# Kernel optimization log

Hardware: AMD Instinct MI355X
Metric: run time of the kernel (lower is better)

The kernel has to match this reference:

```python
import jax, jax.numpy as jnp
import numpy as np

B, S, D, H = 2, 2048, 1024, 16
HD = D // H
NEG = -10000.0


def setup_inputs() -> dict:
    key = jax.random.key(0)
    ks = jax.random.split(key, 9)
    # xavier-uniform-like scale for square d_model x d_model weights
    lim = float(np.sqrt(6.0 / (D + D)))
    mk_w = lambda k: jax.random.uniform(k, (D, D), jnp.float32, -lim, lim)
    return {
        "q": jax.random.normal(ks[0], (B, S, D), jnp.float32),
        "k": jax.random.normal(ks[1], (B, S, D), jnp.float32),
        "v": jax.random.normal(ks[2], (B, S, D), jnp.float32),
        "attn_mask": jax.random.randint(ks[3], (B, S), 0, 2, jnp.int32),
        "Wq": mk_w(ks[4]),
        "Wk": mk_w(ks[5]),
        "Wv": mk_w(ks[6]),
        "Wo": mk_w(ks[7]),
        "mask_future": 1,
    }


def reference(q, k, v, attn_mask, Wq, Wk, Wv, Wo, mask_future):
    # nn.Linear(bias=False): y = x @ W.T
    def split_heads(x, W):
        return (x @ W.T).reshape(B, S, H, HD).transpose(0, 2, 1, 3)  # [B,H,S,HD]

    qh = split_heads(q, Wq)
    kh = split_heads(k, Wk)
    vh = split_heads(v, Wv)

    scale = 1.0 / np.sqrt(HD)
    scores = jnp.einsum("bhld,bhsd->bhls", qh, kh) * scale  # [B,H,L,S]

    if mask_future:  # static python flag
        rows = jnp.arange(S)[:, None]
        cols = jnp.arange(S)[None, :]
        causal_bias = jnp.where(cols > rows, jnp.float32(NEG), jnp.float32(0.0))
        scores = scores + causal_bias

    # masked_fill(attn_mask == 0, -10000): sets score exactly to NEG (after bias add)
    pad = attn_mask[:, None, None, :]  # [B,1,1,S]
    scores = jnp.where(pad == 0, jnp.float32(NEG), scores)

    probs = jax.nn.softmax(scores, axis=-1)
    ctx = jnp.einsum("bhls,bhsd->bhld", probs, vh)  # [B,H,L,HD]
    ctx = ctx.transpose(0, 2, 1, 3).reshape(B, S, D)
    return ctx @ Wo.T
```

## Files before the change

kernel.cpp:

```cpp
#include <hip/hip_runtime.h>
#include <hip/hip_bf16.h>

typedef __attribute__((ext_vector_type(8))) short bf16x8;
typedef __attribute__((ext_vector_type(4))) short bf16x4;
typedef __attribute__((ext_vector_type(4))) float f32x4;

#define B_ 2
#define S_ 2048
#define D_ 1024
#define H_ 16
#define HD_ 64
#define M_ 4096
#define NEGV (-10000.0f)

#define NQ_ 4194304
#define NW_ 1048576

#if __has_builtin(__builtin_amdgcn_mfma_f32_16x16x16bf16_1k)
#define HAVE_MFMA16 1
#else
#define HAVE_MFMA16 0
#endif

static __device__ __forceinline__ unsigned short f2bf(float x) {
  __hip_bfloat16 h = __float2bfloat16(x);
  return *reinterpret_cast<unsigned short*>(&h);
}

static __device__ __forceinline__ bf16x8 cvt8(const float* p) {
  float4 a = *reinterpret_cast<const float4*>(p);
  float4 b = *reinterpret_cast<const float4*>(p + 4);
  bf16x8 r;
  r[0] = (short)f2bf(a.x); r[1] = (short)f2bf(a.y);
  r[2] = (short)f2bf(a.z); r[3] = (short)f2bf(a.w);
  r[4] = (short)f2bf(b.x); r[5] = (short)f2bf(b.y);
  r[6] = (short)f2bf(b.z); r[7] = (short)f2bf(b.w);
  return r;
}

static __device__ __forceinline__ void gl_lds16(const unsigned short* g, unsigned short* l) {
#if __has_builtin(__builtin_amdgcn_global_load_lds)
  __builtin_amdgcn_global_load_lds(
      (const __attribute__((address_space(1))) unsigned int*)g,
      (__attribute__((address_space(3))) unsigned int*)l, 16, 0, 0);
#else
  *reinterpret_cast<bf16x8*>(l) = *reinterpret_cast<const bf16x8*>(g);
#endif
}


__global__ __launch_bounds__(256) void cvt_all(const float* __restrict__ q,
                                               const float* __restrict__ k,
                                               const float* __restrict__ v,
                                               const float* __restrict__ wq,
                                               const float* __restrict__ wk,
                                               const float* __restrict__ wv,
                                               const float* __restrict__ wo,
                                               unsigned short* __restrict__ dst) {
  for (size_t c = (size_t)blockIdx.x * 256 + threadIdx.x; c < 2097152; c += (size_t)2048 * 256) {
    const size_t e = c * 8;
    const float* s;
    if (e < (size_t)NQ_)            s = q  + e;
    else if (e < (size_t)2 * NQ_)   s = k  + (e - (size_t)NQ_);
    else if (e < (size_t)3 * NQ_)   s = v  + (e - (size_t)2 * NQ_);
    else if (e < (size_t)3 * NQ_ + NW_)     s = wq + (e - (size_t)3 * NQ_);
    else if (e < (size_t)3 * NQ_ + 2 * NW_) s = wk + (e - (size_t)3 * NQ_ - NW_);
    else if (e < (size_t)3 * NQ_ + 3 * NW_) s = wv + (e - (size_t)3 * NQ_ - 2 * NW_);
    else                                    s = wo + (e - (size_t)3 * NQ_ - 3 * NW_);
    *reinterpret_cast<bf16x8*>(dst + e) = cvt8(s);
  }
}

template<bool HSPLIT>
static __device__ __forceinline__ void core_fast(const unsigned short* A,
                                                 const unsigned short* Bw,
                                                 unsigned short* Asm, unsigned short* Bsm,
                                                 int m0, int n0, f32x4 (*acc)[4]) {
  const int tid = threadIdx.x, lane = tid & 63, wid = tid >> 6;
  const int wm = wid >> 1, wn = wid & 1;
  const int l15 = lane & 15, l4 = lane >> 4;

  for (int k0 = 0; k0 < 1024; k0 += 64) {
    __syncthreads();
#pragma unroll
    for (int i = 0; i < 4; ++i) {
      const int idx = tid + 256 * i;
      const int row = idx >> 3;
      const int ce = ((idx & 7) * 8) ^ ((row & 7) << 3);
      const unsigned short* ga;
      if constexpr (HSPLIT) {
        const int m = m0 + row, kk = k0 + ce;
        const int bb = m >> 11, s = m & 2047;
        ga = A + (((size_t)(bb * H_ + (kk >> 6)) * S_ + s) * HD_ + (kk & 63));
      } else {
        ga = A + (size_t)(m0 + row) * 1024 + k0 + ce;
      }
      gl_lds16(ga, Asm + (size_t)idx * 8);
      gl_lds16(Bw + (size_t)(n0 + row) * 1024 + k0 + ce, Bsm + (size_t)idx * 8);
    }
    __syncthreads();
#pragma unroll
    for (int kk = 0; kk < 2; ++kk) {
      bf16x8 af[4], bfr[4];
#pragma unroll
      for (int f = 0; f < 4; ++f) {
        const int ra = wm * 64 + f * 16 + l15;
        const int ca = (kk * 32 + l4 * 8) ^ ((ra & 7) << 3);
        af[f] = *reinterpret_cast<const bf16x8*>(&Asm[ra * 64 + ca]);
        const int rb = wn * 64 + f * 16 + l15;
        const int cb = (kk * 32 + l4 * 8) ^ ((rb & 7) << 3);
        bfr[f] = *reinterpret_cast<const bf16x8*>(&Bsm[rb * 64 + cb]);
      }
#pragma unroll
      for (int fm = 0; fm < 4; ++fm)
#pragma unroll
        for (int fn = 0; fn < 4; ++fn)
          acc[fm][fn] = __builtin_amdgcn_mfma_f32_16x16x32_bf16(af[fm], bfr[fn], acc[fm][fn], 0, 0, 0);
    }
  }
}

__global__ __launch_bounds__(256) void gemm_qkv_fast(const unsigned short* __restrict__ qbf,
                                                     const unsigned short* __restrict__ kbf,
                                                     const unsigned short* __restrict__ vbf,
                                                     const unsigned short* __restrict__ wbf,
                                                     unsigned short* __restrict__ Qh,
                                                     unsigned short* __restrict__ Kh,
                                                     unsigned short* __restrict__ Vt) {
  __shared__ unsigned short Asm[128 * 64];
  __shared__ unsigned short Bsm[128 * 64];
  const int z = blockIdx.z;
  const unsigned short* A  = (z == 0) ? qbf : (z == 1) ? kbf : vbf;
  const unsigned short* Bw = wbf + (size_t)z * NW_;
  const int m0 = blockIdx.y * 128, n0 = blockIdx.x * 128;
  const int lane = threadIdx.x & 63, wid = threadIdx.x >> 6;
  const int wm = wid >> 1, wn = wid & 1;
  const int l15 = lane & 15, l4 = lane >> 4;
  f32x4 acc[4][4] = {};
  core_fast<false>(A, Bw, Asm, Bsm, m0, n0, acc);

#pragma unroll
  for (int fm = 0; fm < 4; ++fm) {
#pragma unroll
    for (int fn = 0; fn < 4; ++fn) {
      const int mg0 = m0 + wm * 64 + fm * 16 + l4 * 4;
      const int ng  = n0 + wn * 64 + fn * 16 + l15;
      const int bidx = mg0 >> 11, s = mg0 & 2047;
      const int h = ng >> 6, d = ng & 63;
      if (z < 2) {
        unsigned short* C = (z == 0) ? Qh : Kh;
#pragma unroll
        for (int r = 0; r < 4; ++r)
          C[((size_t)((bidx * H_ + h) * S_ + s + r)) * HD_ + d] = f2bf(acc[fm][fn][r]);
      } else {
        ushort4 pk;
        pk.x = f2bf(acc[fm][fn][0]); pk.y = f2bf(acc[fm][fn][1]);
        pk.z = f2bf(acc[fm][fn][2]); pk.w = f2bf(acc[fm][fn][3]);
        *reinterpret_cast<ushort4*>(&Vt[((size_t)((bidx * H_ + h) * HD_ + d)) * S_ + s]) = pk;
      }
    }
  }
}

__global__ __launch_bounds__(256) void gemm_o_fast(const unsigned short* __restrict__ ctx,
                                                   const unsigned short* __restrict__ wobf,
                                                   float* __restrict__ Cout) {
  __shared__ unsigned short Asm[128 * 64];
  __shared__ unsigned short Bsm[128 * 64];
  const int m0 = blockIdx.y * 128, n0 = blockIdx.x * 128;
  const int lane = threadIdx.x & 63, wid = threadIdx.x >> 6;
  const int wm = wid >> 1, wn = wid & 1;
  const int l15 = lane & 15, l4 = lane >> 4;
  f32x4 acc[4][4] = {};
  core_fast<true>(ctx, wobf, Asm, Bsm, m0, n0, acc);

#pragma unroll
  for (int fm = 0; fm < 4; ++fm)
#pragma unroll
    for (int fn = 0; fn < 4; ++fn) {
      const int mg0 = m0 + wm * 64 + fm * 16 + l4 * 4;
      const int ng  = n0 + wn * 64 + fn * 16 + l15;
#pragma unroll
      for (int r = 0; r < 4; ++r)
        Cout[(size_t)(mg0 + r) * 1024 + ng] = acc[fm][fn][r];
    }
}


template<bool AF32, bool BF32, bool HSPLIT>
static __device__ __forceinline__ void gemm_core(const void* Av, const void* Bv,
                                                 unsigned short* Asm, unsigned short* Bsm,
                                                 int m0, int n0, f32x4 (*acc)[4]) {
  constexpr int BK = 64, LDT = 72;
  constexpr int K = 1024;
  const int tid = threadIdx.x;
  const int lane = tid & 63, wid = tid >> 6;
  const int wm = wid >> 1, wn = wid & 1;
  const int l15 = lane & 15, l4 = lane >> 4;

  for (int k0 = 0; k0 < K; k0 += BK) {
    __syncthreads();
#pragma unroll
    for (int i = 0; i < 4; ++i) {
      int idx = tid + 256 * i;
      int row = idx >> 3, k8 = (idx & 7) * 8;
      bf16x8 va, vb;
      if constexpr (AF32) {
        va = cvt8((const float*)Av + (size_t)(m0 + row) * K + k0 + k8);
      } else if constexpr (HSPLIT) {
        const int m = m0 + row, kk = k0 + k8;
        const int bb = m >> 11, s = m & 2047;
        va = *reinterpret_cast<const bf16x8*>(
            (const unsigned short*)Av +
            (((size_t)(bb * H_ + (kk >> 6)) * S_ + s) * HD_ + (kk & 63)));
      } else {
        va = *reinterpret_cast<const bf16x8*>((const unsigned short*)Av + (size_t)(m0 + row) * K + k0 + k8);
      }
      if constexpr (BF32) {
        vb = cvt8((const float*)Bv + (size_t)(n0 + row) * K + k0 + k8);
      } else {
        vb = *reinterpret_cast<const bf16x8*>((const unsigned short*)Bv + (size_t)(n0 + row) * K + k0 + k8);
      }
      *reinterpret_cast<bf16x8*>(&Asm[row * LDT + k8]) = va;
      *reinterpret_cast<bf16x8*>(&Bsm[row * LDT + k8]) = vb;
    }
    __syncthreads();
#pragma unroll
    for (int kk = 0; kk < 2; ++kk) {
      bf16x8 af[4], bfr[4];
#pragma unroll
      for (int f = 0; f < 4; ++f) {
        af[f]  = *reinterpret_cast<const bf16x8*>(&Asm[(wm * 64 + f * 16 + l15) * LDT + kk * 32 + l4 * 8]);
        bfr[f] = *reinterpret_cast<const bf16x8*>(&Bsm[(wn * 64 + f * 16 + l15) * LDT + kk * 32 + l4 * 8]);
      }
#pragma unroll
      for (int fm = 0; fm < 4; ++fm)
#pragma unroll
        for (int fn = 0; fn < 4; ++fn)
          acc[fm][fn] = __builtin_amdgcn_mfma_f32_16x16x32_bf16(af[fm], bfr[fn], acc[fm][fn], 0, 0, 0);
    }
  }
}

__global__ __launch_bounds__(256) void gemm_qkv3(const float* __restrict__ q,
                                                 const float* __restrict__ k,
                                                 const float* __restrict__ v,
                                                 const float* __restrict__ Wq,
                                                 const float* __restrict__ Wk,
                                                 const float* __restrict__ Wv,
                                                 unsigned short* __restrict__ Qh,
                                                 unsigned short* __restrict__ Kh,
                                                 unsigned short* __restrict__ Vt) {
  constexpr int LDT = 72;
  __shared__ unsigned short Asm[128 * LDT];
  __shared__ unsigned short Bsm[128 * LDT];
  const int z = blockIdx.z;
  const float* A  = (z == 0) ? q  : (z == 1) ? k  : v;
  const float* Bw = (z == 0) ? Wq : (z == 1) ? Wk : Wv;
  const int m0 = blockIdx.y * 128, n0 = blockIdx.x * 128;
  const int lane = threadIdx.x & 63, wid = threadIdx.x >> 6;
  const int wm = wid >> 1, wn = wid & 1;
  const int l15 = lane & 15, l4 = lane >> 4;
  f32x4 acc[4][4] = {};
  gemm_core<true, true, false>(A, Bw, Asm, Bsm, m0, n0, acc);

#pragma unroll
  for (int fm = 0; fm < 4; ++fm) {
#pragma unroll
    for (int fn = 0; fn < 4; ++fn) {
      const int mg0 = m0 + wm * 64 + fm * 16 + l4 * 4;
      const int ng  = n0 + wn * 64 + fn * 16 + l15;
      const int bidx = mg0 >> 11, s = mg0 & 2047;
      const int h = ng >> 6, d = ng & 63;
      if (z < 2) {
        unsigned short* C = (z == 0) ? Qh : Kh;
#pragma unroll
        for (int r = 0; r < 4; ++r)
          C[((size_t)((bidx * H_ + h) * S_ + s + r)) * HD_ + d] = f2bf(acc[fm][fn][r]);
      } else {
        ushort4 pk;
        pk.x = f2bf(acc[fm][fn][0]); pk.y = f2bf(acc[fm][fn][1]);
        pk.z = f2bf(acc[fm][fn][2]); pk.w = f2bf(acc[fm][fn][3]);
        *reinterpret_cast<ushort4*>(&Vt[((size_t)((bidx * H_ + h) * HD_ + d)) * S_ + s]) = pk;
      }
    }
  }
}

__global__ __launch_bounds__(256) void gemm_oproj(const void* __restrict__ Av,
                                                  const void* __restrict__ Bv,
                                                  float* __restrict__ Cout) {
  constexpr int LDT = 72;
  __shared__ unsigned short Asm[128 * LDT];
  __shared__ unsigned short Bsm[128 * LDT];
  const int m0 = blockIdx.y * 128, n0 = blockIdx.x * 128;
  const int lane = threadIdx.x & 63, wid = threadIdx.x >> 6;
  const int wm = wid >> 1, wn = wid & 1;
  const int l15 = lane & 15, l4 = lane >> 4;
  f32x4 acc[4][4] = {};
  gemm_core<false, true, true>(Av, Bv, Asm, Bsm, m0, n0, acc);

#pragma unroll
  for (int fm = 0; fm < 4; ++fm)
#pragma unroll
    for (int fn = 0; fn < 4; ++fn) {
      const int mg0 = m0 + wm * 64 + fm * 16 + l4 * 4;
      const int ng  = n0 + wn * 64 + fn * 16 + l15;
#pragma unroll
      for (int r = 0; r < 4; ++r)
        Cout[(size_t)(mg0 + r) * 1024 + ng] = acc[fm][fn][r];
    }
}

__global__ __launch_bounds__(128) void attn_fwd(const unsigned short* Qh,
                                                const unsigned short* __restrict__ Kh,
                                                const unsigned short* __restrict__ Vt,
                                                const int* __restrict__ attn_mask,
                                                const int* __restrict__ mask_future,
                                                unsigned short* ctx) {
  constexpr int KVB = 64;
  constexpr int LDK = 72;
  constexpr int LDV = 72;
  __shared__ unsigned short Ksm[KVB * LDK];
  __shared__ unsigned short Vsm[64 * LDV];
#if !HAVE_MFMA16
  __shared__ unsigned short Psm[2][16 * LDV];
#endif
  __shared__ int s_any;
  const int tid = threadIdx.x, lane = tid & 63, wid = tid >> 6;
  const int l15 = lane & 15, l4 = lane >> 4;
  const int bh = blockIdx.y, b = bh >> 4;
  const int q0t = (int)((blockIdx.x + 9 * blockIdx.y) & 63);
  const int q0 = q0t * 32;
  const bool causal = (mask_future[0] != 0);

  if (tid == 0) s_any = 0;
  __syncthreads();
  for (int i = tid; i <= q0; i += 128)
    if (attn_mask[b * S_ + i]) s_any = 1;
  __syncthreads();
  const int kb_end = (causal && s_any) ? (q0 + 32) : S_;

  const unsigned short* Qb = Qh + (size_t)bh * S_ * HD_;
  const unsigned short* Kb = Kh + (size_t)bh * S_ * HD_;
  const unsigned short* Vb = Vt + (size_t)bh * HD_ * S_;
  const int* mrow = attn_mask + b * S_;

  const int qrow = q0 + wid * 16 + l15;
  const bf16x8 qf0 = *reinterpret_cast<const bf16x8*>(&Qb[(size_t)qrow * HD_ + l4 * 8]);
  const bf16x8 qf1 = *reinterpret_cast<const bf16x8*>(&Qb[(size_t)qrow * HD_ + 32 + l4 * 8]);

  float m_run = -1e30f, l_run = 0.f;
  f32x4 o[4] = {};

  bf16x8 kreg[4], vreg[4];
#pragma unroll
  for (int j = 0; j < 4; ++j) {
    const int idx = tid + 128 * j;
    kreg[j] = *reinterpret_cast<const bf16x8*>(&Kb[(size_t)(idx >> 3) * HD_ + (idx & 7) * 8]);
    vreg[j] = *reinterpret_cast<const bf16x8*>(&Vb[(size_t)(idx >> 3) * S_ + (idx & 7) * 8]);
  }

  for (int kb = 0; kb < kb_end; kb += KVB) {
    __syncthreads();
#pragma unroll
    for (int j = 0; j < 4; ++j) {
      const int idx = tid + 128 * j;
      *reinterpret_cast<bf16x8*>(&Ksm[(idx >> 3) * LDK + (idx & 7) * 8]) = kreg[j];
      *reinterpret_cast<bf16x8*>(&Vsm[(idx >> 3) * LDV + (idx & 7) * 8]) = vreg[j];
    }
    __syncthreads();

    if (kb + KVB < kb_end) {
      const int kn = kb + KVB;
#pragma unroll
      for (int j = 0; j < 4; ++j) {
        const int idx = tid + 128 * j;
        kreg[j] = *reinterpret_cast<const bf16x8*>(&Kb[(size_t)(kn + (idx >> 3)) * HD_ + (idx & 7) * 8]);
        vreg[j] = *reinterpret_cast<const bf16x8*>(&Vb[(size_t)(idx >> 3) * S_ + kn + (idx & 7) * 8]);
      }
    }

    f32x4 sc[4];
#pragma unroll
    for (int nf = 0; nf < 4; ++nf) {
      bf16x8 kf0 = *reinterpret_cast<const bf16x8*>(&Ksm[(nf * 16 + l15) * LDK + l4 * 8]);
      bf16x8 kf1 = *reinterpret_cast<const bf16x8*>(&Ksm[(nf * 16 + l15) * LDK + 32 + l4 * 8]);
      f32x4 z = {};
      z = __builtin_amdgcn_mfma_f32_16x16x32_bf16(kf0, qf0, z, 0, 0, 0);
      z = __builtin_amdgcn_mfma_f32_16x16x32_bf16(kf1, qf1, z, 0, 0, 0);
      sc[nf] = z;
    }

    float p[4][4];
    float mx = -1e30f;
#pragma unroll
    for (int nf = 0; nf < 4; ++nf) {
      const int4 mk4 = *reinterpret_cast<const int4*>(&mrow[kb + nf * 16 + l4 * 4]);
      const int kbase = kb + nf * 16 + l4 * 4;
#pragma unroll
      for (int r = 0; r < 4; ++r) {
        float vv = sc[nf][r] * 0.125f;
        if (causal && (kbase + r) > qrow) vv += NEGV;
        const int mkr = (r == 0) ? mk4.x : (r == 1) ? mk4.y : (r == 2) ? mk4.z : mk4.w;
        if (mkr == 0) vv = NEGV;
        p[nf][r] = vv;
        mx = fmaxf(mx, vv);
      }
    }
    mx = fmaxf(mx, __shfl_xor(mx, 16));
    mx = fmaxf(mx, __shfl_xor(mx, 32));
    const float m_new = fmaxf(m_run, mx);
    const float scale = __expf(m_run - m_new);
    float s_loc = 0.f;
#pragma unroll
    for (int nf = 0; nf < 4; ++nf)
#pragma unroll
      for (int r = 0; r < 4; ++r) {
        float e = __expf(p[nf][r] - m_new);
        p[nf][r] = e;
        s_loc += e;
      }
    s_loc += __shfl_xor(s_loc, 16);
    s_loc += __shfl_xor(s_loc, 32);
    l_run = l_run * scale + s_loc;
    m_run = m_new;

    float sq[4];
#pragma unroll
    for (int r = 0; r < 4; ++r) sq[r] = __shfl(scale, l4 * 4 + r);
#pragma unroll
    for (int nf2 = 0; nf2 < 4; ++nf2)
#pragma unroll
      for (int r = 0; r < 4; ++r) o[nf2][r] *= sq[r];

#if HAVE_MFMA16
    bf16x4 pk[4];
#pragma unroll
    for (int nf = 0; nf < 4; ++nf) {
      bf16x4 t;
      t[0] = (short)f2bf(p[nf][0]); t[1] = (short)f2bf(p[nf][1]);
      t[2] = (short)f2bf(p[nf][2]); t[3] = (short)f2bf(p[nf][3]);
      pk[nf] = t;
    }
#pragma unroll
    for (int nf2 = 0; nf2 < 4; ++nf2) {
#pragma unroll
      for (int nf = 0; nf < 4; ++nf) {
        bf16x4 vf = *reinterpret_cast<const bf16x4*>(&Vsm[(nf2 * 16 + l15) * LDV + nf * 16 + l4 * 4]);
        o[nf2] = __builtin_amdgcn_mfma_f32_16x16x16bf16_1k(pk[nf], vf, o[nf2], 0, 0, 0);
      }
    }
#else
    unsigned short* Pw = &Psm[wid][0];
#pragma unroll
    for (int nf = 0; nf < 4; ++nf)
#pragma unroll
      for (int r = 0; r < 4; ++r)
        Pw[l15 * LDV + nf * 16 + l4 * 4 + r] = f2bf(p[nf][r]);
#pragma unroll
    for (int nf2 = 0; nf2 < 4; ++nf2) {
#pragma unroll
      for (int kk = 0; kk < 2; ++kk) {
        bf16x8 pf = *reinterpret_cast<const bf16x8*>(&Pw[l15 * LDV + kk * 32 + l4 * 8]);
        bf16x8 vf = *reinterpret_cast<const bf16x8*>(&Vsm[(nf2 * 16 + l15) * LDV + kk * 32 + l4 * 8]);
        o[nf2] = __builtin_amdgcn_mfma_f32_16x16x32_bf16(pf, vf, o[nf2], 0, 0, 0);
      }
    }
#endif
  }

  const float linv = 1.f / l_run;
  float lq[4];
#pragma unroll
  for (int r = 0; r < 4; ++r) lq[r] = __shfl(linv, l4 * 4 + r);
#pragma unroll
  for (int nf2 = 0; nf2 < 4; ++nf2)
#pragma unroll
    for (int r = 0; r < 4; ++r) {
      const int rowg = q0 + wid * 16 + l4 * 4 + r;
      ctx[((size_t)bh * S_ + rowg) * HD_ + nf2 * 16 + l15] = f2bf(o[nf2][r] * lq[r]);
    }
}

extern "C" void kernel_launch(void* const* d_in, const int* in_sizes, int n_in,
                              void* d_out, int out_size, void* d_ws, size_t ws_size,
                              hipStream_t stream) {
  const float* q = (const float*)d_in[0];
  const float* k = (const float*)d_in[1];
  const float* v = (const float*)d_in[2];
  const int* attn_mask = (const int*)d_in[3];
  const float* Wq = (const float*)d_in[4];
  const float* Wk = (const float*)d_in[5];
  const float* Wv = (const float*)d_in[6];
  const float* Wo = (const float*)d_in[7];
  const int* mask_future = (const int*)d_in[8];

  unsigned short* ws = (unsigned short*)d_ws;
  unsigned short* Vt = (unsigned short*)d_out;
  float* out = (float*)d_out;
  (void)in_sizes; (void)n_in; (void)out_size;

  const size_t CVT_ELEMS = (size_t)3 * NQ_ + 4 * NW_;
  const size_t NEED = (CVT_ELEMS + 2 * (size_t)NQ_) * 2;

  if (ws_size >= NEED) {
    unsigned short* cvt = ws;
    unsigned short* qbf = cvt;
    unsigned short* kbf = cvt + (size_t)NQ_;
    unsigned short* vbf = cvt + (size_t)2 * NQ_;
    unsigned short* wbf = cvt + (size_t)3 * NQ_;
    unsigned short* Qh  = cvt + CVT_ELEMS;
    unsigned short* Kh  = Qh + (size_t)NQ_;

    cvt_all<<<2048, 256, 0, stream>>>(q, k, v, Wq, Wk, Wv, Wo, cvt);
    gemm_qkv_fast<<<dim3(8, 32, 3), 256, 0, stream>>>(qbf, kbf, vbf, wbf, Qh, Kh, Vt);
    attn_fwd<<<dim3(64, 32), 128, 0, stream>>>(Qh, Kh, Vt, attn_mask, mask_future, Qh);
    gemm_o_fast<<<dim3(8, 32), 256, 0, stream>>>(Qh, wbf + (size_t)3 * NW_, out);
  } else {
    unsigned short* Qh = ws;
    unsigned short* Kh = ws + (size_t)NQ_;
    gemm_qkv3<<<dim3(8, 32, 3), 256, 0, stream>>>(q, k, v, Wq, Wk, Wv, Qh, Kh, Vt);
    attn_fwd<<<dim3(64, 32), 128, 0, stream>>>(Qh, Kh, Vt, attn_mask, mask_future, Qh);
    gemm_oproj<<<dim3(8, 32), 256, 0, stream>>>(Qh, Wo, out);
  }
}
```

Baseline: 173.2 us.

## Pair causal query tiles per block and XOR-swizzle K/V shared memory

Each attention block now handles two query tiles, bx and 63-bx, so every block does about the same amount of causal work, and the grid is halved. The padded K/V shared-memory tiles are replaced by unpadded 64x64 tiles with an XOR swizzle applied to the global load columns and to the fragment reads, to avoid bank conflicts without padding. The cost is fewer blocks in flight, serialized tiles within a block, and extra barriers between the halves.

After: 212.7 us. +22.8%, slower.

```diff
diff --git a/kernel.cpp b/kernel.cpp
--- a/kernel.cpp
+++ b/kernel.cpp
@@ -319,168 +319,177 @@
                                                 const int* __restrict__ mask_future,
                                                 unsigned short* ctx) {
   constexpr int KVB = 64;
-  constexpr int LDK = 72;
-  constexpr int LDV = 72;
-  __shared__ unsigned short Ksm[KVB * LDK];
-  __shared__ unsigned short Vsm[64 * LDV];
+  __shared__ unsigned short Ksm[64 * 64];
+  __shared__ unsigned short Vsm[64 * 64];
 #if !HAVE_MFMA16
-  __shared__ unsigned short Psm[2][16 * LDV];
+  __shared__ unsigned short Psm[2][16 * 72];
 #endif
   __shared__ int s_any;
   const int tid = threadIdx.x, lane = tid & 63, wid = tid >> 6;
   const int l15 = lane & 15, l4 = lane >> 4;
   const int bh = blockIdx.y, b = bh >> 4;
-  const int q0t = (int)((blockIdx.x + 9 * blockIdx.y) & 63);
-  const int q0 = q0t * 32;
+  const int bx = (int)blockIdx.x;
   const bool causal = (mask_future[0] != 0);
-
-  if (tid == 0) s_any = 0;
-  __syncthreads();
-  for (int i = tid; i <= q0; i += 128)
-    if (attn_mask[b * S_ + i]) s_any = 1;
-  __syncthreads();
-  const int kb_end = (causal && s_any) ? (q0 + 32) : S_;
 
   const unsigned short* Qb = Qh + (size_t)bh * S_ * HD_;
   const unsigned short* Kb = Kh + (size_t)bh * S_ * HD_;
   const unsigned short* Vb = Vt + (size_t)bh * HD_ * S_;
   const int* mrow = attn_mask + b * S_;
 
-  const int qrow = q0 + wid * 16 + l15;
-  const bf16x8 qf0 = *reinterpret_cast<const bf16x8*>(&Qb[(size_t)qrow * HD_ + l4 * 8]);
-  const bf16x8 qf1 = *reinterpret_cast<const bf16x8*>(&Qb[(size_t)qrow * HD_ + 32 + l4 * 8]);
-
-  float m_run = -1e30f, l_run = 0.f;
-  f32x4 o[4] = {};
-
-  bf16x8 kreg[4], vreg[4];
-#pragma unroll
-  for (int j = 0; j < 4; ++j) {
-    const int idx = tid + 128 * j;
-    kreg[j] = *reinterpret_cast<const bf16x8*>(&Kb[(size_t)(idx >> 3) * HD_ + (idx & 7) * 8]);
-    vreg[j] = *reinterpret_cast<const bf16x8*>(&Vb[(size_t)(idx >> 3) * S_ + (idx & 7) * 8]);
-  }
-
-  for (int kb = 0; kb < kb_end; kb += KVB) {
-    __syncthreads();
+  for (int half = 0; half < 2; ++half) {
+    const int q0 = (half ? (63 - bx) : bx) * 32;
+
+    __syncthreads();
+    if (tid == 0) s_any = 0;
+    __syncthreads();
+    for (int i = tid; i <= q0; i += 128)
+      if (mrow[i]) s_any = 1;
+    __syncthreads();
+    const int kb_end = (causal && s_any) ? (q0 + 32) : S_;
+
+    const int qrow = q0 + wid * 16 + l15;
+    const bf16x8 qf0 = *reinterpret_cast<const bf16x8*>(&Qb[(size_t)qrow * HD_ + l4 * 8]);
+    const bf16x8 qf1 = *reinterpret_cast<const bf16x8*>(&Qb[(size_t)qrow * HD_ + 32 + l4 * 8]);
+
+    float m_run = -1e30f, l_run = 0.f;
+    f32x4 o[4] = {};
+
+    bf16x8 kreg[4], vreg[4];
 #pragma unroll
     for (int j = 0; j < 4; ++j) {
       const int idx = tid + 128 * j;
-      *reinterpret_cast<bf16x8*>(&Ksm[(idx >> 3) * LDK + (idx & 7) * 8]) = kreg[j];
-      *reinterpret_cast<bf16x8*>(&Vsm[(idx >> 3) * LDV + (idx & 7) * 8]) = vreg[j];
-    }
-    __syncthreads();
-
-    if (kb + KVB < kb_end) {
-      const int kn = kb + KVB;
+      const int row = idx >> 3;
+      const int ce = ((idx & 7) * 8) ^ ((row & 7) << 3);
+      kreg[j] = *reinterpret_cast<const bf16x8*>(&Kb[(size_t)row * HD_ + ce]);
+      vreg[j] = *reinterpret_cast<const bf16x8*>(&Vb[(size_t)row * S_ + ce]);
+    }
+
+    for (int kb = 0; kb < kb_end; kb += KVB) {
+      __syncthreads();
 #pragma unroll
       for (int j = 0; j < 4; ++j) {
         const int idx = tid + 128 * j;
-        kreg[j] = *reinterpret_cast<const bf16x8*>(&Kb[(size_t)(kn + (idx >> 3)) * HD_ + (idx & 7) * 8]);
-        vreg[j] = *reinterpret_cast<const bf16x8*>(&Vb[(size_t)(idx >> 3) * S_ + kn + (idx & 7) * 8]);
-      }
-    }
-
-    f32x4 sc[4];
-#pragma unroll
-    for (int nf = 0; nf < 4; ++nf) {
-      bf16x8 kf0 = *reinterpret_cast<const bf16x8*>(&Ksm[(nf * 16 + l15) * LDK + l4 * 8]);
-      bf16x8 kf1 = *reinterpret_cast<const bf16x8*>(&Ksm[(nf * 16 + l15) * LDK + 32 + l4 * 8]);
-      f32x4 z = {};
-      z = __builtin_amdgcn_mfma_f32_16x16x32_bf16(kf0, qf0, z, 0, 0, 0);
-      z = __builtin_amdgcn_mfma_f32_16x16x32_bf16(kf1, qf1, z, 0, 0, 0);
-      sc[nf] = z;
-    }
-
-    float p[4][4];
-    float mx = -1e30f;
-#pragma unroll
-    for (int nf = 0; nf < 4; ++nf) {
-      const int4 mk4 = *reinterpret_cast<const int4*>(&mrow[kb + nf * 16 + l4 * 4]);
-      const int kbase = kb + nf * 16 + l4 * 4;
+        *reinterpret_cast<bf16x8*>(&Ksm[idx * 8]) = kreg[j];
+        *reinterpret_cast<bf16x8*>(&Vsm[idx * 8]) = vreg[j];
+      }
+      __syncthreads();
+
+      if (kb + KVB < kb_end) {
+        const int kn = kb + KVB;
+#pragma unroll
+        for (int j = 0; j < 4; ++j) {
+          const int idx = tid + 128 * j;
+          const int row = idx >> 3;
+          const int ce = ((idx & 7) * 8) ^ ((row & 7) << 3);
+          kreg[j] = *reinterpret_cast<const bf16x8*>(&Kb[(size_t)(kn + row) * HD_ + ce]);
+          vreg[j] = *reinterpret_cast<const bf16x8*>(&Vb[(size_t)row * S_ + kn + ce]);
+        }
+      }
+
+      f32x4 sc[4];
+#pragma unroll
+      for (int nf = 0; nf < 4; ++nf) {
+        const int ra = nf * 16 + l15, sw = (ra & 7) << 3;
+        bf16x8 kf0 = *reinterpret_cast<const bf16x8*>(&Ksm[ra * 64 + ((l4 * 8) ^ sw)]);
+        bf16x8 kf1 = *reinterpret_cast<const bf16x8*>(&Ksm[ra * 64 + ((32 + l4 * 8) ^ sw)]);
+        f32x4 z = {};
+        z = __builtin_amdgcn_mfma_f32_16x16x32_bf16(kf0, qf0, z, 0, 0, 0);
+        z = __builtin_amdgcn_mfma_f32_16x16x32_bf16(kf1, qf1, z, 0, 0, 0);
+        sc[nf] = z;
+      }
+
+      float p[4][4];
+      float mx = -1e30f;
+#pragma unroll
+      for (int nf = 0; nf < 4; ++nf) {
+        const int4 mk4 = *reinterpret_cast<const int4*>(&mrow[kb + nf * 16 + l4 * 4]);
+        const int kbase = kb + nf * 16 + l4 * 4;
+#pragma unroll
+        for (int r = 0; r < 4; ++r) {
+          float vv = sc[nf][r] * 0.125f;
+          if (causal && (kbase + r) > qrow) vv += NEGV;
+          const int mkr = (r == 0) ? mk4.x : (r == 1) ? mk4.y : (r == 2) ? mk4.z : mk4.w;
+          if (mkr == 0) vv = NEGV;
+          p[nf][r] = vv;
+          mx = fmaxf(mx, vv);
+        }
+      }
+      mx = fmaxf(mx, __shfl_xor(mx, 16));
+      mx = fmaxf(mx, __shfl_xor(mx, 32));
+      const float m_new = fmaxf(m_run, mx);
+      const float scale = __expf(m_run - m_new);
+      float s_loc = 0.f;
+#pragma unroll
+      for (int nf = 0; nf < 4; ++nf)
+#pragma unroll
+        for (int r = 0; r < 4; ++r) {
+          float e = __expf(p[nf][r] - m_new);
+          p[nf][r] = e;
+          s_loc += e;
+        }
+      s_loc += __shfl_xor(s_loc, 16);
+      s_loc += __shfl_xor(s_loc, 32);
+      l_run = l_run * scale + s_loc;
+      m_run = m_new;
+
+      float sq[4];
+#pragma unroll
+      for (int r = 0; r < 4; ++r) sq[r] = __shfl(scale, l4 * 4 + r);
+#pragma unroll
+      for (int nf2 = 0; nf2 < 4; ++nf2)
+#pragma unroll
+        for (int r = 0; r < 4; ++r) o[nf2][r] *= sq[r];
+
+#if HAVE_MFMA16
+      bf16x4 pk[4];
+#pragma unroll
+      for (int nf = 0; nf < 4; ++nf) {
+        bf16x4 t;
+        t[0] = (short)f2bf(p[nf][0]); t[1] = (short)f2bf(p[nf][1]);
+        t[2] = (short)f2bf(p[nf][2]); t[3] = (short)f2bf(p[nf][3]);
+        pk[nf] = t;
+      }
+#pragma unroll
+      for (int nf2 = 0; nf2 < 4; ++nf2) {
+        const int rv = nf2 * 16 + l15, swv = (rv & 7) << 3;
+#pragma unroll
+        for (int nf = 0; nf < 4; ++nf) {
+          bf16x4 vf = *reinterpret_cast<const bf16x4*>(&Vsm[rv * 64 + ((nf * 16 + l4 * 4) ^ swv)]);
+          o[nf2] = __builtin_amdgcn_mfma_f32_16x16x16bf16_1k(pk[nf], vf, o[nf2], 0, 0, 0);
+        }
+      }
+#else
+      unsigned short* Pw = &Psm[wid][0];
+#pragma unroll
+      for (int nf = 0; nf < 4; ++nf)
+#pragma unroll
+        for (int r = 0; r < 4; ++r)
+          Pw[l15 * 72 + nf * 16 + l4 * 4 + r] = f2bf(p[nf][r]);
+#pragma unroll
+      for (int nf2 = 0; nf2 < 4; ++nf2) {
+        const int rv = nf2 * 16 + l15, swv = (rv & 7) << 3;
+#pragma unroll
+        for (int kk = 0; kk < 2; ++kk) {
+          bf16x8 pf = *reinterpret_cast<const bf16x8*>(&Pw[l15 * 72 + kk * 32 + l4 * 8]);
+          bf16x8 vf = *reinterpret_cast<const bf16x8*>(&Vsm[rv * 64 + ((kk * 32 + l4 * 8) ^ swv)]);
+          o[nf2] = __builtin_amdgcn_mfma_f32_16x16x32_bf16(pf, vf, o[nf2], 0, 0, 0);
+        }
+      }
+#endif
+    }
+
+    const float linv = 1.f / l_run;
+    float lq[4];
+#pragma unroll
+    for (int r = 0; r < 4; ++r) lq[r] = __shfl(linv, l4 * 4 + r);
+#pragma unroll
+    for (int nf2 = 0; nf2 < 4; ++nf2)
 #pragma unroll
       for (int r = 0; r < 4; ++r) {
-        float vv = sc[nf][r] * 0.125f;
-        if (causal && (kbase + r) > qrow) vv += NEGV;
-        const int mkr = (r == 0) ? mk4.x : (r == 1) ? mk4.y : (r == 2) ? mk4.z : mk4.w;
-        if (mkr == 0) vv = NEGV;
-        p[nf][r] = vv;
-        mx = fmaxf(mx, vv);
-      }
-    }
-    mx = fmaxf(mx, __shfl_xor(mx, 16));
-    mx = fmaxf(mx, __shfl_xor(mx, 32));
-    const float m_new = fmaxf(m_run, mx);
-    const float scale = __expf(m_run - m_new);
-    float s_loc = 0.f;
-#pragma unroll
-    for (int nf = 0; nf < 4; ++nf)
-#pragma unroll
-      for (int r = 0; r < 4; ++r) {
-        float e = __expf(p[nf][r] - m_new);
-        p[nf][r] = e;
-        s_loc += e;
-      }
-    s_loc += __shfl_xor(s_loc, 16);
-    s_loc += __shfl_xor(s_loc, 32);
-    l_run = l_run * scale + s_loc;
-    m_run = m_new;
-
-    float sq[4];
-#pragma unroll
-    for (int r = 0; r < 4; ++r) sq[r] = __shfl(scale, l4 * 4 + r);
-#pragma unroll
-    for (int nf2 = 0; nf2 < 4; ++nf2)
-#pragma unroll
-      for (int r = 0; r < 4; ++r) o[nf2][r] *= sq[r];
-
-#if HAVE_MFMA16
-    bf16x4 pk[4];
-#pragma unroll
-    for (int nf = 0; nf < 4; ++nf) {
-      bf16x4 t;
-      t[0] = (short)f2bf(p[nf][0]); t[1] = (short)f2bf(p[nf][1]);
-      t[2] = (short)f2bf(p[nf][2]); t[3] = (short)f2bf(p[nf][3]);
-      pk[nf] = t;
-    }
-#pragma unroll
-    for (int nf2 = 0; nf2 < 4; ++nf2) {
-#pragma unroll
-      for (int nf = 0; nf < 4; ++nf) {
-        bf16x4 vf = *reinterpret_cast<const bf16x4*>(&Vsm[(nf2 * 16 + l15) * LDV + nf * 16 + l4 * 4]);
-        o[nf2] = __builtin_amdgcn_mfma_f32_16x16x16bf16_1k(pk[nf], vf, o[nf2], 0, 0, 0);
-      }
-    }
-#else
-    unsigned short* Pw = &Psm[wid][0];
-#pragma unroll
-    for (int nf = 0; nf < 4; ++nf)
-#pragma unroll
-      for (int r = 0; r < 4; ++r)
-        Pw[l15 * LDV + nf * 16 + l4 * 4 + r] = f2bf(p[nf][r]);
-#pragma unroll
-    for (int nf2 = 0; nf2 < 4; ++nf2) {
-#pragma unroll
-      for (int kk = 0; kk < 2; ++kk) {
-        bf16x8 pf = *reinterpret_cast<const bf16x8*>(&Pw[l15 * LDV + kk * 32 + l4 * 8]);
-        bf16x8 vf = *reinterpret_cast<const bf16x8*>(&Vsm[(nf2 * 16 + l15) * LDV + kk * 32 + l4 * 8]);
-        o[nf2] = __builtin_amdgcn_mfma_f32_16x16x32_bf16(pf, vf, o[nf2], 0, 0, 0);
-      }
-    }
-#endif
-  }
-
-  const float linv = 1.f / l_run;
-  float lq[4];
-#pragma unroll
-  for (int r = 0; r < 4; ++r) lq[r] = __shfl(linv, l4 * 4 + r);
-#pragma unroll
-  for (int nf2 = 0; nf2 < 4; ++nf2)
-#pragma unroll
-    for (int r = 0; r < 4; ++r) {
-      const int rowg = q0 + wid * 16 + l4 * 4 + r;
-      ctx[((size_t)bh * S_ + rowg) * HD_ + nf2 * 16 + l15] = f2bf(o[nf2][r] * lq[r]);
-    }
+        const int rowg = q0 + wid * 16 + l4 * 4 + r;
+        ctx[((size_t)bh * S_ + rowg) * HD_ + nf2 * 16 + l15] = f2bf(o[nf2][r] * lq[r]);
+      }
+  }
 }
 
 extern "C" void kernel_launch(void* const* d_in, const int* in_sizes, int n_in,
@@ -515,13 +524,13 @@
 
     cvt_all<<<2048, 256, 0, stream>>>(q, k, v, Wq, Wk, Wv, Wo, cvt);
     gemm_qkv_fast<<<dim3(8, 32, 3), 256, 0, stream>>>(qbf, kbf, vbf, wbf, Qh, Kh, Vt);
-    attn_fwd<<<dim3(64, 32), 128, 0, stream>>>(Qh, Kh, Vt, attn_mask, mask_future, Qh);
+    attn_fwd<<<dim3(32, 32), 128, 0, stream>>>(Qh, Kh, Vt, attn_mask, mask_future, Qh);
     gemm_o_fast<<<dim3(8, 32), 256, 0, stream>>>(Qh, wbf + (size_t)3 * NW_, out);
   } else {
     unsigned short* Qh = ws;
     unsigned short* Kh = ws + (size_t)NQ_;
     gemm_qkv3<<<dim3(8, 32, 3), 256, 0, stream>>>(q, k, v, Wq, Wk, Wv, Qh, Kh, Vt);
-    attn_fwd<<<dim3(64, 32), 128, 0, stream>>>(Qh, Kh, Vt, attn_mask, mask_future, Qh);
+    attn_fwd<<<dim3(32, 32), 128, 0, stream>>>(Qh, Kh, Vt, attn_mask, mask_future, Qh);
     gemm_oproj<<<dim3(8, 32), 256, 0, stream>>>(Qh, Wo, out);
   }
 }
```
